# Kernel tuning notes

Hardware: AMD Instinct MI355X
Metric: run time of the kernel (lower is better)

Reference implementation:

```python
import jax, jax.numpy as jnp
import numpy as np

N_NODES = 200000
N_GRAPHS = 512

def gcn_conv(x, src, dst, W, b):
    # PyG GCNConv: add self-loops, symmetric normalization, linear, scatter-add
    n = x.shape[0]
    loop = jnp.arange(n)
    s = jnp.concatenate([src, loop])
    d = jnp.concatenate([dst, loop])
    deg = jax.ops.segment_sum(jnp.ones_like(d, dtype=x.dtype), d, num_segments=n)
    dinv = jnp.where(deg > 0, jax.lax.rsqrt(deg), 0.0)
    norm = dinv[s] * dinv[d]                      # [E+n]
    h = x @ W                                     # [n, out]
    msg = h[s] * norm[:, None]                    # gather on source nodes
    return jax.ops.segment_sum(msg, d, num_segments=n) + b

def setup_inputs() -> dict:
    key = jax.random.key(0)
    ks = jax.random.split(key, 24)
    def g(i, shape, scale=0.05):
        return jax.random.normal(ks[i], shape, dtype=jnp.float32) * scale
    inp = {}
    inp['x'] = jax.random.normal(ks[0], (N_NODES, 78), dtype=jnp.float32)
    inp['edge_index'] = jax.random.randint(ks[1], (2, 800000), 0, N_NODES)
    inp['batch'] = jnp.sort(jax.random.randint(ks[2], (N_NODES,), 0, N_GRAPHS))
    inp['target'] = jax.random.randint(ks[3], (N_GRAPHS, 1000), 0, 26)
    inp['W1'] = g(4, (78, 78)); inp['b1'] = jnp.zeros((78,), jnp.float32)
    inp['W2'] = g(5, (78, 156)); inp['b2'] = jnp.zeros((156,), jnp.float32)
    inp['W3'] = g(6, (156, 312)); inp['b3'] = jnp.zeros((312,), jnp.float32)
    inp['Wg1'] = g(7, (312, 1024)); inp['bg1'] = jnp.zeros((1024,), jnp.float32)
    inp['Wg2'] = g(8, (1024, 128)); inp['bg2'] = jnp.zeros((128,), jnp.float32)
    inp['emb'] = g(9, (26, 128), 1.0)
    inp['convw'] = g(10, (32, 1000, 8))  # OIW
    inp['convb'] = jnp.zeros((32,), jnp.float32)
    inp['Wxt'] = g(11, (32 * 121, 128)); inp['bxt'] = jnp.zeros((128,), jnp.float32)
    inp['Wf1'] = g(12, (256, 1024)); inp['bf1'] = jnp.zeros((1024,), jnp.float32)
    inp['Wf2'] = g(13, (1024, 512)); inp['bf2'] = jnp.zeros((512,), jnp.float32)
    inp['Wo'] = g(14, (512, 1)); inp['bo'] = jnp.zeros((1,), jnp.float32)
    return inp

def reference(x, edge_index, batch, target, W1, b1, W2, b2, W3, b3,
              Wg1, bg1, Wg2, bg2, emb, convw, convb, Wxt, bxt,
              Wf1, bf1, Wf2, bf2, Wo, bo):
    src, dst = edge_index[0], edge_index[1]
    h = jax.nn.relu(gcn_conv(x, src, dst, W1, b1))
    h = jax.nn.relu(gcn_conv(h, src, dst, W2, b2))
    h = jax.nn.relu(gcn_conv(h, src, dst, W3, b3))          # [N, 312]
    g = jax.ops.segment_max(h, batch, num_segments=N_GRAPHS)  # [B, 312]
    g = jnp.where(jnp.isfinite(g), g, 0.0)                   # guard empty segments
    g = jax.nn.relu(g @ Wg1 + bg1)                            # dropout = identity (eval)
    g = g @ Wg2 + bg2                                         # [B, 128]

    e = emb[target]                                           # [B, 1000, 128]
    c = jax.lax.conv_general_dilated(e, convw, (1,), 'VALID',
                                     dimension_numbers=('NCW', 'OIW', 'NCW'))
    c = c + convb[None, :, None]                              # [B, 32, 121]
    xt = c.reshape(-1, 32 * 121) @ Wxt + bxt                  # [B, 128]

    xc = jnp.concatenate([g, xt], axis=1)                     # [B, 256]
    xc = jax.nn.relu(xc @ Wf1 + bf1)
    xc = jax.nn.relu(xc @ Wf2 + bf2)
    return xc @ Wo + bo                                       # [B, 1]
```

## Files before the change

### kernel.cpp

```cpp
#include <hip/hip_runtime.h>
#include <hip/hip_bf16.h>

#define N_NODES 200000
#define N_EDGES 800000
#define N_GRAPHS 512

typedef __attribute__((ext_vector_type(8))) short short8v;
typedef __attribute__((ext_vector_type(4))) float f32x4;
typedef __attribute__((ext_vector_type(2))) float f32x2;
typedef __attribute__((ext_vector_type(2))) unsigned int u32x2;
typedef __attribute__((ext_vector_type(4))) unsigned int u32x4;
typedef __attribute__((ext_vector_type(4))) int i32x4;

__device__ inline float bf2f(unsigned int u) {
    union { unsigned int i; float f; } c;
    c.i = u << 16;
    return c.f;
}
__device__ inline unsigned short f2bf(float f) {
    union { __hip_bfloat16 h; unsigned short u; } c;
    c.h = __float2bfloat16(f);
    return c.u;
}


__global__ __launch_bounds__(256) void count_edges(const int* __restrict__ dst, int E,
                                                   int* __restrict__ cnt) {
    int e = blockIdx.x * 256 + threadIdx.x;
    if (e < E) atomicAdd(&cnt[dst[e]], 1);
}

__global__ __launch_bounds__(512) void block_reduce(const int* __restrict__ in, int n,
                                                    int* __restrict__ bsum) {
    __shared__ int s[512];
    int i = blockIdx.x * 512 + threadIdx.x;
    s[threadIdx.x] = (i < n) ? in[i] : 0;
    __syncthreads();
    for (int off = 256; off; off >>= 1) {
        if (threadIdx.x < off) s[threadIdx.x] += s[threadIdx.x + off];
        __syncthreads();
    }
    if (threadIdx.x == 0) bsum[blockIdx.x] = s[0];
}

__global__ __launch_bounds__(512) void scan_bsums(int* bsum, int nb) {
    __shared__ int buf[2][512];
    int t = threadIdx.x;
    int v = (t < nb) ? bsum[t] : 0;
    buf[0][t] = v;
    __syncthreads();
    int src = 0;
    for (int off = 1; off < 512; off <<= 1) {
        int x = buf[src][t];
        if (t >= off) x += buf[src][t - off];
        buf[src ^ 1][t] = x;
        src ^= 1;
        __syncthreads();
    }
    if (t < nb) bsum[t] = buf[src][t] - v;
}

__global__ __launch_bounds__(512) void block_scan_write(const int* __restrict__ cnt,
                                                        const int* __restrict__ bsum, int n,
                                                        int* __restrict__ rowptr) {
    __shared__ int buf[2][512];
    int t = threadIdx.x;
    int i = blockIdx.x * 512 + t;
    int v = (i < n) ? cnt[i] : 0;
    buf[0][t] = v;
    __syncthreads();
    int src = 0;
    for (int off = 1; off < 512; off <<= 1) {
        int x = buf[src][t];
        if (t >= off) x += buf[src][t - off];
        buf[src ^ 1][t] = x;
        src ^= 1;
        __syncthreads();
    }
    int incl = buf[src][t];
    int base = bsum[blockIdx.x];
    if (i < n) rowptr[i] = base + incl - v;
    if (i == n - 1) rowptr[n] = base + incl;
}

__global__ __launch_bounds__(256) void fill_csr(const int* __restrict__ src,
                                                const int* __restrict__ dst, int E,
                                                const int* __restrict__ rowptr,
                                                int* __restrict__ cur, int* __restrict__ col) {
    int e = blockIdx.x * 256 + threadIdx.x;
    if (e < E) {
        int d = dst[e];
        int p = atomicAdd(&cur[d], 1);
        col[rowptr[d] + p] = src[e];
    }
}

__global__ __launch_bounds__(256) void compute_dinv(const int* __restrict__ rowptr, int n,
                                                    float* __restrict__ dinv) {
    int v = blockIdx.x * 256 + threadIdx.x;
    if (v < n) {
        int deg = rowptr[v + 1] - rowptr[v] + 1;
        dinv[v] = rsqrtf((float)deg);
    }
}

__global__ __launch_bounds__(64) void graph_bounds(const int* __restrict__ batch, int n, int ng,
                                                   int* __restrict__ gstart) {
    int b = blockIdx.x * 64 + threadIdx.x;
    if (b > ng) return;
    if (b == ng) { gstart[ng] = n; return; }
    int lo = 0, hi = n;
    while (lo < hi) {
        int mid = (lo + hi) >> 1;
        if (batch[mid] < b) lo = mid + 1; else hi = mid;
    }
    gstart[b] = lo;
}


__global__ __launch_bounds__(256) void scale_x(const float* __restrict__ x,
                                               const float* __restrict__ dinv,
                                               unsigned short* __restrict__ XS) {
    int idx = blockIdx.x * 256 + threadIdx.x;
    int v = idx / 40, c = idx % 40;
    if (v >= N_NODES) return;
    if (c == 39) {
        *(unsigned int*)(XS + (size_t)v * 80 + 78) = 0u;
        return;
    }
    float dv = dinv[v];
    f32x2 xv = *(const f32x2*)(x + (size_t)v * 78 + c * 2);
    unsigned int pack = ((unsigned int)f2bf(xv.y * dv) << 16) | f2bf(xv.x * dv);
    *(unsigned int*)(XS + (size_t)v * 80 + c * 2) = pack;
}


template <int LD, int NCH, int NPB>
__global__ __launch_bounds__(256) void agg_sum(const unsigned short* __restrict__ X,
                                               const float* __restrict__ dinv,
                                               const int* __restrict__ rowptr,
                                               const int* __restrict__ col,
                                               unsigned short* __restrict__ out) {
    int tid = threadIdx.x;
    if (tid >= NPB * NCH) return;
    int v = blockIdx.x * NPB + tid / NCH;
    int c = tid % NCH;
    if (v >= N_NODES) return;
    u32x4 xv = *(const u32x4*)(X + (size_t)v * LD + c * 8);
    float a0 = bf2f(xv.x & 0xffffu), a1 = bf2f(xv.x >> 16);
    float a2 = bf2f(xv.y & 0xffffu), a3 = bf2f(xv.y >> 16);
    float a4 = bf2f(xv.z & 0xffffu), a5 = bf2f(xv.z >> 16);
    float a6 = bf2f(xv.w & 0xffffu), a7 = bf2f(xv.w >> 16);
    int r0 = rowptr[v], r1 = rowptr[v + 1];
    for (int e = r0; e < r1; ++e) {
        int u = col[e];
        u32x4 xu = *(const u32x4*)(X + (size_t)u * LD + c * 8);
        a0 += bf2f(xu.x & 0xffffu);
        a1 += bf2f(xu.x >> 16);
        a2 += bf2f(xu.y & 0xffffu);
        a3 += bf2f(xu.y >> 16);
        a4 += bf2f(xu.z & 0xffffu);
        a5 += bf2f(xu.z >> 16);
        a6 += bf2f(xu.w & 0xffffu);
        a7 += bf2f(xu.w >> 16);
    }
    float dv = dinv[v];
    u32x4 o;
    o.x = ((unsigned int)f2bf(a1 * dv) << 16) | f2bf(a0 * dv);
    o.y = ((unsigned int)f2bf(a3 * dv) << 16) | f2bf(a2 * dv);
    o.z = ((unsigned int)f2bf(a5 * dv) << 16) | f2bf(a4 * dv);
    o.w = ((unsigned int)f2bf(a7 * dv) << 16) | f2bf(a6 * dv);
    *(u32x4*)(out + (size_t)v * LD + c * 8) = o;
}


template <int KREAL, int NREAL, int KS, int NF>
__global__ __launch_bounds__(256) void prep_wf(const float* __restrict__ W,
                                               unsigned short* __restrict__ Wf) {
    int idx = blockIdx.x * 256 + threadIdx.x;
    if (idx >= NF * KS * 64) return;
    int lane = idx & 63, ks = (idx >> 6) % KS, nf = idx / (64 * KS);
    int k0 = ks * 32 + 8 * (lane >> 4);
    int cc = nf * 16 + (lane & 15);
    short8v t;
#pragma unroll
    for (int j = 0; j < 8; j++) {
        int k = k0 + j;
        float w = (k < KREAL && cc < NREAL) ? W[(size_t)k * NREAL + cc] : 0.f;
        t[j] = (short)f2bf(w);
    }
    *(short8v*)&Wf[(size_t)idx * 8] = t;
}


template <int NREAL, int LDA, int LDC, int NF, int KS>
__global__ __launch_bounds__(256) void gemm_mfma_node(const unsigned short* __restrict__ A,
                                                      const unsigned short* __restrict__ Wf,
                                                      const float* __restrict__ bias,
                                                      const float* __restrict__ dinv,
                                                      unsigned short* __restrict__ Cout, int M) {
    __shared__ unsigned short Bs[NF * KS * 64 * 8];
    int tid = threadIdx.x;
    for (int idx = tid; idx < NF * KS * 64; idx += 256)
        *(short8v*)&Bs[idx * 8] = *(const short8v*)&Wf[(size_t)idx * 8];
    __syncthreads();

    int lane = tid & 63, wid = tid >> 6;
    int m0 = blockIdx.x * 128 + wid * 32;
    float biasr[NF];
#pragma unroll
    for (int nf = 0; nf < NF; nf++) {
        int cc = nf * 16 + (lane & 15);
        biasr[nf] = (cc < NREAL) ? bias[cc] : 0.f;
    }
    f32x4 acc[2][NF];
#pragma unroll
    for (int mf = 0; mf < 2; mf++)
#pragma unroll
        for (int nf = 0; nf < NF; nf++) acc[mf][nf] = (f32x4){0.f, 0.f, 0.f, 0.f};

    int ra = min(m0 + (lane & 15), M - 1);
    int rb = min(m0 + 16 + (lane & 15), M - 1);
#pragma unroll
    for (int ks = 0; ks < KS; ks++) {
        int koff = ks * 32 + 8 * (lane >> 4);
        short8v a0 = *(const short8v*)(A + (size_t)ra * LDA + koff);
        short8v a1 = *(const short8v*)(A + (size_t)rb * LDA + koff);
#pragma unroll
        for (int nf = 0; nf < NF; nf++) {
            short8v b = *(const short8v*)&Bs[((nf * KS + ks) * 64 + lane) * 8];
            acc[0][nf] = __builtin_amdgcn_mfma_f32_16x16x32_bf16(a0, b, acc[0][nf], 0, 0, 0);
            acc[1][nf] = __builtin_amdgcn_mfma_f32_16x16x32_bf16(a1, b, acc[1][nf], 0, 0, 0);
        }
    }
    float dr[2][4];
#pragma unroll
    for (int mf = 0; mf < 2; mf++)
#pragma unroll
        for (int r = 0; r < 4; r++) {
            int row = m0 + mf * 16 + 4 * (lane >> 4) + r;
            dr[mf][r] = dinv[min(row, M - 1)];
        }
#pragma unroll
    for (int mf = 0; mf < 2; mf++) {
#pragma unroll
        for (int nf = 0; nf < NF; nf++) {
            int cc = nf * 16 + (lane & 15);
#pragma unroll
            for (int r = 0; r < 4; r++) {
                int row = m0 + mf * 16 + 4 * (lane >> 4) + r;
                float v = fmaxf(acc[mf][nf][r] + biasr[nf], 0.f) * dr[mf][r];
                unsigned short o = (cc < NREAL) ? f2bf(v) : (unsigned short)0;
                if (row < M) Cout[(size_t)row * LDC + cc] = o;
            }
        }
    }
}


__global__ __launch_bounds__(256) void seg_gemm_max(const unsigned short* __restrict__ A,
                                                    const unsigned short* __restrict__ Wf3,
                                                    const float* __restrict__ b3,
                                                    const int* __restrict__ gstart,
                                                    float* __restrict__ g3) {
    __shared__ unsigned short Bs[4 * 5 * 64 * 8];
    __shared__ float wmax[4][64];
    int g = blockIdx.x & 511;
    int bx = blockIdx.x >> 9;
    int c0 = bx * 64;
    int r0 = gstart[g], r1 = gstart[g + 1];
    int tid = threadIdx.x, lane = tid & 63, wid = tid >> 6;

    const unsigned short* src = Wf3 + (size_t)bx * 4 * 5 * 64 * 8;
    for (int idx = tid; idx < 1280; idx += 256)
        *(short8v*)&Bs[idx * 8] = *(const short8v*)&src[(size_t)idx * 8];
    __syncthreads();

    float biasr[4], cmax[4];
#pragma unroll
    for (int nf = 0; nf < 4; nf++) {
        int cc = c0 + nf * 16 + (lane & 15);
        biasr[nf] = (cc < 312) ? b3[cc] : 0.f;
        cmax[nf] = 0.f;
    }

    for (int mt = r0 + wid * 32; mt < r1; mt += 128) {
        f32x4 acc[2][4];
#pragma unroll
        for (int mf = 0; mf < 2; mf++)
#pragma unroll
            for (int nf = 0; nf < 4; nf++) acc[mf][nf] = (f32x4){0.f, 0.f, 0.f, 0.f};
        int ra = min(mt + (lane & 15), N_NODES - 1);
        int rb = min(mt + 16 + (lane & 15), N_NODES - 1);
#pragma unroll
        for (int ks = 0; ks < 5; ks++) {
            int koff = ks * 32 + 8 * (lane >> 4);
            short8v a0 = *(const short8v*)(A + (size_t)ra * 160 + koff);
            short8v a1 = *(const short8v*)(A + (size_t)rb * 160 + koff);
#pragma unroll
            for (int nf = 0; nf < 4; nf++) {
                short8v b = *(const short8v*)&Bs[((nf * 5 + ks) * 64 + lane) * 8];
                acc[0][nf] = __builtin_amdgcn_mfma_f32_16x16x32_bf16(a0, b, acc[0][nf], 0, 0, 0);
                acc[1][nf] = __builtin_amdgcn_mfma_f32_16x16x32_bf16(a1, b, acc[1][nf], 0, 0, 0);
            }
        }
#pragma unroll
        for (int mf = 0; mf < 2; mf++) {
#pragma unroll
            for (int nf = 0; nf < 4; nf++) {
#pragma unroll
                for (int r = 0; r < 4; r++) {
                    int row = mt + mf * 16 + 4 * (lane >> 4) + r;
                    float v = fmaxf(acc[mf][nf][r] + biasr[nf], 0.f);
                    if (row < r1) cmax[nf] = fmaxf(cmax[nf], v);
                }
            }
        }
    }
#pragma unroll
    for (int nf = 0; nf < 4; nf++) {
        float m = cmax[nf];
        m = fmaxf(m, __shfl_xor(m, 16));
        m = fmaxf(m, __shfl_xor(m, 32));
        if (lane < 16) wmax[wid][nf * 16 + lane] = m;
    }
    __syncthreads();
    if (tid < 64) {
        float m = fmaxf(fmaxf(wmax[0][tid], wmax[1][tid]), fmaxf(wmax[2][tid], wmax[3][tid]));
        int cc = c0 + tid;
        if (cc < 312) g3[(size_t)g * 312 + cc] = m;
    }
}


__global__ __launch_bounds__(256) void init_bias_all(float* __restrict__ gg,
                                                     const float* __restrict__ bg1,
                                                     float* __restrict__ xc,
                                                     const float* __restrict__ bg2,
                                                     const float* __restrict__ bxt,
                                                     float* __restrict__ f1,
                                                     const float* __restrict__ bf1,
                                                     float* __restrict__ f2,
                                                     const float* __restrict__ bf2) {
    int idx = blockIdx.x * 256 + threadIdx.x;
    int row = idx / 2816, c = idx % 2816;
    if (row >= N_GRAPHS) return;
    if (c < 1024) gg[(size_t)row * 1024 + c] = bg1[c];
    else if (c < 1280) {
        int j = c - 1024;
        xc[(size_t)row * 256 + j] = (j < 128) ? bg2[j] : bxt[j - 128];
    } else if (c < 2304)
        f1[(size_t)row * 1024 + (c - 1280)] = bf1[c - 1280];
    else
        f2[(size_t)row * 512 + (c - 2304)] = bf2[c - 2304];
}

template <int RELUA>
__global__ __launch_bounds__(256) void gemm_splitk(const float* __restrict__ A,
                                                   const float* __restrict__ B,
                                                   float* __restrict__ C, int M, int N, int K,
                                                   int ldc, int Kc) {
    __shared__ float As[16][17];
    __shared__ float Bs[16][64];
    int bx = blockIdx.x, by = blockIdx.y, bz = blockIdx.z;
    int tid = threadIdx.x;
    int lane = tid & 63, wy = tid >> 6;
    int n0 = bx * 64, m0 = by * 16;
    int k0 = bz * Kc, k1 = min(K, k0 + Kc);
    float acc[4] = {0.f, 0.f, 0.f, 0.f};
    for (int kt = k0; kt < k1; kt += 16) {
        {
            int r = tid >> 4, kk = tid & 15;
            int gm = m0 + r, gk = kt + kk;
            float v = (gk < k1 && gm < M) ? A[(size_t)gm * K + gk] : 0.f;
            if (RELUA) v = fmaxf(v, 0.f);
            As[kk][r] = v;
        }
#pragma unroll
        for (int l = 0; l < 4; l++) {
            int kk = wy + l * 4;
            int gk = kt + kk, gn = n0 + lane;
            Bs[kk][lane] = (gk < k1 && gn < N) ? B[(size_t)gk * N + gn] : 0.f;
        }
        __syncthreads();
#pragma unroll
        for (int kk = 0; kk < 16; kk++) {
            float b = Bs[kk][lane];
#pragma unroll
            for (int r = 0; r < 4; r++) acc[r] += As[kk][wy * 4 + r] * b;
        }
        __syncthreads();
    }
    int gn = n0 + lane;
    if (gn < N) {
#pragma unroll
        for (int r = 0; r < 4; r++) {
            int gm = m0 + wy * 4 + r;
            if (gm < M) atomicAdd(&C[(size_t)gm * ldc + gn], acc[r]);
        }
    }
}


__global__ __launch_bounds__(256) void prep_cwf(const float* __restrict__ convw,
                                                unsigned short* __restrict__ CWf) {
    int idx = blockIdx.x * 256 + threadIdx.x;
    int ks = idx >> 10, nf = (idx >> 6) & 15, lane = idx & 63;
    int k0 = ks * 32 + 8 * (lane >> 4);
    int c = nf * 16 + (lane & 15);
    int o = c >> 3, kk = c & 7;
    short8v t;
#pragma unroll
    for (int j = 0; j < 8; j++) {
        int k = k0 + j;
        float v = (k < 1000) ? convw[(size_t)o * 8000 + k * 8 + kk] : 0.f;
        t[j] = (short)f2bf(v);
    }
    *(short8v*)&CWf[(size_t)idx * 8] = t;
}

__global__ __launch_bounds__(256) void prep_ef(const float* __restrict__ emb,
                                               unsigned short* __restrict__ Ef) {
    int idx = blockIdx.x * 256 + threadIdx.x;
    if (idx >= 7 * 8 * 64) return;
    int ks = idx >> 9, nf = (idx >> 6) & 7, lane = idx & 63;
    int j0 = ks * 32 + 8 * (lane >> 4);
    int w = nf * 16 + (lane & 15);
    short8v t;
#pragma unroll
    for (int j8 = 0; j8 < 8; j8++) {
        int j = j0 + j8;
        float v = (j < 208 && w < 121) ? emb[(size_t)(j >> 3) * 128 + w + (j & 7)] : 0.f;
        t[j8] = (short)f2bf(v);
    }
    *(short8v*)&Ef[(size_t)idx * 8] = t;
}

__global__ __launch_bounds__(256) void conv_mfma(const int* __restrict__ target,
                                                 const unsigned short* __restrict__ CWf,
                                                 const unsigned short* __restrict__ Ef,
                                                 const float* __restrict__ convb,
                                                 float* __restrict__ c) {
    __shared__ int tg[1024];
    __shared__ unsigned short A_lds[32 * 256];
    int n = blockIdx.x;
    int tid = threadIdx.x, lane = tid & 63, wid = tid >> 6;
    int hi = lane >> 4, l15 = lane & 15;
    for (int i = tid; i < 1024; i += 256) tg[i] = (i < 1000) ? target[n * 1000 + i] : -1;
    __syncthreads();

    f32x4 acc[2][4];
#pragma unroll
    for (int mf = 0; mf < 2; mf++)
#pragma unroll
        for (int nf = 0; nf < 4; nf++) acc[mf][nf] = (f32x4){0.f, 0.f, 0.f, 0.f};
    int r0 = l15, r1 = l15 + 16;
    for (int ks = 0; ks < 32; ks++) {
        int kk = ks * 32 + 8 * hi;
        i32x4 ta = *(const i32x4*)&tg[kk];
        i32x4 tb = *(const i32x4*)&tg[kk + 4];
        short8v a0, a1;
        a0[0] = (ta.x == r0) ? (short)0x3F80 : (short)0;
        a0[1] = (ta.y == r0) ? (short)0x3F80 : (short)0;
        a0[2] = (ta.z == r0) ? (short)0x3F80 : (short)0;
        a0[3] = (ta.w == r0) ? (short)0x3F80 : (short)0;
        a0[4] = (tb.x == r0) ? (short)0x3F80 : (short)0;
        a0[5] = (tb.y == r0) ? (short)0x3F80 : (short)0;
        a0[6] = (tb.z == r0) ? (short)0x3F80 : (short)0;
        a0[7] = (tb.w == r0) ? (short)0x3F80 : (short)0;
        a1[0] = (ta.x == r1) ? (short)0x3F80 : (short)0;
        a1[1] = (ta.y == r1) ? (short)0x3F80 : (short)0;
        a1[2] = (ta.z == r1) ? (short)0x3F80 : (short)0;
        a1[3] = (ta.w == r1) ? (short)0x3F80 : (short)0;
        a1[4] = (tb.x == r1) ? (short)0x3F80 : (short)0;
        a1[5] = (tb.y == r1) ? (short)0x3F80 : (short)0;
        a1[6] = (tb.z == r1) ? (short)0x3F80 : (short)0;
        a1[7] = (tb.w == r1) ? (short)0x3F80 : (short)0;
#pragma unroll
        for (int nf = 0; nf < 4; nf++) {
            short8v b = *(const short8v*)&CWf[((size_t)(ks * 16 + wid * 4 + nf) * 64 + lane) * 8];
            acc[0][nf] = __builtin_amdgcn_mfma_f32_16x16x32_bf16(a0, b, acc[0][nf], 0, 0, 0);
            acc[1][nf] = __builtin_amdgcn_mfma_f32_16x16x32_bf16(a1, b, acc[1][nf], 0, 0, 0);
        }
    }
#pragma unroll
    for (int mf = 0; mf < 2; mf++)
#pragma unroll
        for (int nf = 0; nf < 4; nf++) {
            int col = (wid * 4 + nf) * 16 + l15;
#pragma unroll
            for (int r = 0; r < 4; r++) {
                int row = 16 * mf + 4 * hi + r;
                A_lds[row * 256 + col] = f2bf(acc[mf][nf][r]);
            }
        }
    __syncthreads();

    f32x4 acc2[2][2];
#pragma unroll
    for (int mf = 0; mf < 2; mf++)
#pragma unroll
        for (int nf = 0; nf < 2; nf++) acc2[mf][nf] = (f32x4){0.f, 0.f, 0.f, 0.f};
#pragma unroll
    for (int ks = 0; ks < 7; ks++) {
        int j0 = ks * 32 + 8 * hi;
        int t = j0 >> 3;
        short8v a0 = *(const short8v*)&A_lds[t * 256 + l15 * 8];
        short8v a1 = *(const short8v*)&A_lds[t * 256 + (l15 + 16) * 8];
#pragma unroll
        for (int nf = 0; nf < 2; nf++) {
            short8v b = *(const short8v*)&Ef[((size_t)(ks * 8 + wid * 2 + nf) * 64 + lane) * 8];
            acc2[0][nf] = __builtin_amdgcn_mfma_f32_16x16x32_bf16(a0, b, acc2[0][nf], 0, 0, 0);
            acc2[1][nf] = __builtin_amdgcn_mfma_f32_16x16x32_bf16(a1, b, acc2[1][nf], 0, 0, 0);
        }
    }
#pragma unroll
    for (int mf = 0; mf < 2; mf++)
#pragma unroll
        for (int nf = 0; nf < 2; nf++) {
            int w = (wid * 2 + nf) * 16 + l15;
            if (w < 121) {
#pragma unroll
                for (int r = 0; r < 4; r++) {
                    int o = 16 * mf + 4 * hi + r;
                    c[(size_t)n * 3872 + o * 121 + w] = acc2[mf][nf][r] + convb[o];
                }
            }
        }
}


__global__ __launch_bounds__(256) void rowdot(const float* __restrict__ f2,
                                              const float* __restrict__ Wo,
                                              const float* __restrict__ bo,
                                              float* __restrict__ out, int M, int K) {
    int row = blockIdx.x * 4 + (threadIdx.x >> 6);
    int lane = threadIdx.x & 63;
    if (row >= M) return;
    float acc = 0.f;
    for (int k = lane; k < K; k += 64) acc += fmaxf(f2[(size_t)row * K + k], 0.f) * Wo[k];
    for (int off = 32; off; off >>= 1) acc += __shfl_down(acc, off);
    if (lane == 0) out[row] = acc + bo[0];
}


extern "C" void kernel_launch(void* const* d_in, const int* in_sizes, int n_in, void* d_out,
                              int out_size, void* d_ws, size_t ws_size, hipStream_t stream) {
    const float* x = (const float*)d_in[0];
    const int* ei = (const int*)d_in[1];
    const int* batch = (const int*)d_in[2];
    const int* target = (const int*)d_in[3];
    const float* W1 = (const float*)d_in[4];
    const float* b1 = (const float*)d_in[5];
    const float* W2 = (const float*)d_in[6];
    const float* b2 = (const float*)d_in[7];
    const float* W3 = (const float*)d_in[8];
    const float* b3 = (const float*)d_in[9];
    const float* Wg1 = (const float*)d_in[10];
    const float* bg1 = (const float*)d_in[11];
    const float* Wg2 = (const float*)d_in[12];
    const float* bg2 = (const float*)d_in[13];
    const float* emb = (const float*)d_in[14];
    const float* convw = (const float*)d_in[15];
    const float* convb = (const float*)d_in[16];
    const float* Wxt = (const float*)d_in[17];
    const float* bxt = (const float*)d_in[18];
    const float* Wf1 = (const float*)d_in[19];
    const float* bf1 = (const float*)d_in[20];
    const float* Wf2 = (const float*)d_in[21];
    const float* bf2 = (const float*)d_in[22];
    const float* Wo = (const float*)d_in[23];
    const float* bo = (const float*)d_in[24];
    float* out = (float*)d_out;

    const int N = N_NODES, E = N_EDGES;
    const int NB = (N + 511) / 512;

    char* ws = (char*)d_ws;
    size_t off = 0;
    auto alloc = [&](size_t bytes) -> char* {
        char* p = ws + off;
        off = (off + bytes + 255) & ~(size_t)255;
        return p;
    };
    int* cnt = (int*)alloc((size_t)N * 2 * 4);
    int* cur = cnt + N;
    int* rowptr = (int*)alloc((size_t)(N + 1) * 4);
    int* bsum = (int*)alloc(512 * 4);
    int* col = (int*)alloc((size_t)E * 4);
    float* dinv = (float*)alloc((size_t)N * 4);
    int* gstart = (int*)alloc((N_GRAPHS + 1) * 4);
    float* g3 = (float*)alloc((size_t)N_GRAPHS * 312 * 4);
    float* gg = (float*)alloc((size_t)N_GRAPHS * 1024 * 4);
    float* cbuf = (float*)alloc((size_t)N_GRAPHS * 3872 * 4);
    float* xc = (float*)alloc((size_t)N_GRAPHS * 256 * 4);
    float* f1 = (float*)alloc((size_t)N_GRAPHS * 1024 * 4);
    float* f2 = (float*)alloc((size_t)N_GRAPHS * 512 * 4);
    unsigned short* CWf = (unsigned short*)alloc((size_t)32768 * 8 * 2);
    unsigned short* Ef = (unsigned short*)alloc((size_t)3584 * 8 * 2);
    unsigned short* W1f = (unsigned short*)alloc((size_t)5 * 3 * 64 * 8 * 2);
    unsigned short* W2f = (unsigned short*)alloc((size_t)10 * 3 * 64 * 8 * 2);
    unsigned short* W3f = (unsigned short*)alloc((size_t)20 * 5 * 64 * 8 * 2);
    unsigned short* U = (unsigned short*)alloc((size_t)N * 160 * 2 + 512);
    unsigned short* P160 = (unsigned short*)alloc((size_t)N * 160 * 2 + 512);
    unsigned short* H1 = U + (size_t)N * 80;

    const int* srcp = ei;
    const int* dstp = ei + E;

    hipMemsetAsync(cnt, 0, (size_t)N * 2 * 4, stream);
    count_edges<<<(E + 255) / 256, 256, 0, stream>>>(dstp, E, cnt);
    block_reduce<<<NB, 512, 0, stream>>>(cnt, N, bsum);
    scan_bsums<<<1, 512, 0, stream>>>(bsum, NB);
    block_scan_write<<<NB, 512, 0, stream>>>(cnt, bsum, N, rowptr);
    fill_csr<<<(E + 255) / 256, 256, 0, stream>>>(srcp, dstp, E, rowptr, cur, col);
    compute_dinv<<<(N + 255) / 256, 256, 0, stream>>>(rowptr, N, dinv);
    graph_bounds<<<(N_GRAPHS + 1 + 63) / 64, 64, 0, stream>>>(batch, N, N_GRAPHS, gstart);

    init_bias_all<<<(N_GRAPHS * 2816 + 255) / 256, 256, 0, stream>>>(gg, bg1, xc, bg2, bxt, f1,
                                                                     bf1, f2, bf2);
    prep_cwf<<<128, 256, 0, stream>>>(convw, CWf);
    prep_ef<<<14, 256, 0, stream>>>(emb, Ef);
    prep_wf<78, 78, 3, 5><<<4, 256, 0, stream>>>(W1, W1f);
    prep_wf<78, 156, 3, 10><<<8, 256, 0, stream>>>(W2, W2f);
    prep_wf<156, 312, 5, 20><<<25, 256, 0, stream>>>(W3, W3f);

    const int MB = (N + 127) / 128;

    scale_x<<<(N * 40 + 255) / 256, 256, 0, stream>>>(x, dinv, P160);
    agg_sum<80, 10, 25><<<(N + 24) / 25, 256, 0, stream>>>(P160, dinv, rowptr, col, U);
    gemm_mfma_node<78, 80, 80, 5, 3><<<MB, 256, 0, stream>>>(U, W1f, b1, dinv, H1, N);
    agg_sum<80, 10, 25><<<(N + 24) / 25, 256, 0, stream>>>(H1, dinv, rowptr, col, P160);
    gemm_mfma_node<156, 80, 160, 10, 3><<<MB, 256, 0, stream>>>(P160, W2f, b2, dinv, U, N);
    agg_sum<160, 20, 12><<<(N + 11) / 12, 256, 0, stream>>>(U, dinv, rowptr, col, P160);
    seg_gemm_max<<<5 * N_GRAPHS, 256, 0, stream>>>(P160, W3f, b3, gstart, g3);

    gemm_splitk<0><<<dim3(16, 32, 2), 256, 0, stream>>>(g3, Wg1, gg, 512, 1024, 312, 1024, 160);
    gemm_splitk<1><<<dim3(2, 32, 8), 256, 0, stream>>>(gg, Wg2, xc, 512, 128, 1024, 256, 128);

    conv_mfma<<<N_GRAPHS, 256, 0, stream>>>(target, CWf, Ef, convb, cbuf);
    gemm_splitk<0><<<dim3(2, 32, 16), 256, 0, stream>>>(cbuf, Wxt, xc + 128, 512, 128, 3872, 256, 256);

    gemm_splitk<0><<<dim3(16, 32, 2), 256, 0, stream>>>(xc, Wf1, f1, 512, 1024, 256, 1024, 128);
    gemm_splitk<1><<<dim3(8, 32, 8), 256, 0, stream>>>(f1, Wf2, f2, 512, 512, 1024, 512, 128);
    rowdot<<<(N_GRAPHS + 3) / 4, 256, 0, stream>>>(f2, Wo, bo, out, N_GRAPHS, 512);
}
```

Measured before the change: 690.8 us.

## Merge setup kernels and unroll neighbor aggregation with dual accumulators

```diff
diff --git a/kernel.cpp b/kernel.cpp
--- a/kernel.cpp
+++ b/kernel.cpp
@@ -43,7 +43,22 @@
     if (threadIdx.x == 0) bsum[blockIdx.x] = s[0];
 }
 
-__global__ __launch_bounds__(512) void scan_bsums(int* bsum, int nb) {
+__global__ __launch_bounds__(512) void scan_and_bounds(int* bsum, int nb,
+                                                       const int* __restrict__ batch, int n,
+                                                       int ng, int* __restrict__ gstart) {
+    if (blockIdx.x == 1) {
+        int b = threadIdx.x;
+        if (b == 0) gstart[ng] = n;
+        if (b < ng) {
+            int lo = 0, hi = n;
+            while (lo < hi) {
+                int mid = (lo + hi) >> 1;
+                if (batch[mid] < b) lo = mid + 1; else hi = mid;
+            }
+            gstart[b] = lo;
+        }
+        return;
+    }
     __shared__ int buf[2][512];
     int t = threadIdx.x;
     int v = (t < nb) ? bsum[t] : 0;
@@ -62,7 +77,8 @@
 
 __global__ __launch_bounds__(512) void block_scan_write(const int* __restrict__ cnt,
                                                         const int* __restrict__ bsum, int n,
-                                                        int* __restrict__ rowptr) {
+                                                        int* __restrict__ rowptr,
+                                                        float* __restrict__ dinv) {
     __shared__ int buf[2][512];
     int t = threadIdx.x;
     int i = blockIdx.x * 512 + t;
@@ -79,7 +95,10 @@
     }
     int incl = buf[src][t];
     int base = bsum[blockIdx.x];
-    if (i < n) rowptr[i] = base + incl - v;
+    if (i < n) {
+        rowptr[i] = base + incl - v;
+        dinv[i] = rsqrtf((float)(v + 1));
+    }
     if (i == n - 1) rowptr[n] = base + incl;
 }
 
@@ -93,28 +112,6 @@
         int p = atomicAdd(&cur[d], 1);
         col[rowptr[d] + p] = src[e];
     }
-}
-
-__global__ __launch_bounds__(256) void compute_dinv(const int* __restrict__ rowptr, int n,
-                                                    float* __restrict__ dinv) {
-    int v = blockIdx.x * 256 + threadIdx.x;
-    if (v < n) {
-        int deg = rowptr[v + 1] - rowptr[v] + 1;
-        dinv[v] = rsqrtf((float)deg);
-    }
-}
-
-__global__ __launch_bounds__(64) void graph_bounds(const int* __restrict__ batch, int n, int ng,
-                                                   int* __restrict__ gstart) {
-    int b = blockIdx.x * 64 + threadIdx.x;
-    if (b > ng) return;
-    if (b == ng) { gstart[ng] = n; return; }
-    int lo = 0, hi = n;
-    while (lo < hi) {
-        int mid = (lo + hi) >> 1;
-        if (batch[mid] < b) lo = mid + 1; else hi = mid;
-    }
-    gstart[b] = lo;
 }
 
 
@@ -146,38 +143,60 @@
     int v = blockIdx.x * NPB + tid / NCH;
     int c = tid % NCH;
     if (v >= N_NODES) return;
-    u32x4 xv = *(const u32x4*)(X + (size_t)v * LD + c * 8);
+    const unsigned short* Xc = X + c * 8;
+    u32x4 xv = *(const u32x4*)(Xc + (size_t)v * LD);
     float a0 = bf2f(xv.x & 0xffffu), a1 = bf2f(xv.x >> 16);
     float a2 = bf2f(xv.y & 0xffffu), a3 = bf2f(xv.y >> 16);
     float a4 = bf2f(xv.z & 0xffffu), a5 = bf2f(xv.z >> 16);
     float a6 = bf2f(xv.w & 0xffffu), a7 = bf2f(xv.w >> 16);
+    float b0 = 0.f, b1 = 0.f, b2 = 0.f, b3 = 0.f, b4 = 0.f, b5 = 0.f, b6 = 0.f, b7 = 0.f;
     int r0 = rowptr[v], r1 = rowptr[v + 1];
-    for (int e = r0; e < r1; ++e) {
+    int e = r0;
+    for (; e + 1 < r1; e += 2) {
+        int u0 = col[e], u1 = col[e + 1];
+        u32x4 p = *(const u32x4*)(Xc + (size_t)u0 * LD);
+        u32x4 q = *(const u32x4*)(Xc + (size_t)u1 * LD);
+        a0 += bf2f(p.x & 0xffffu);
+        a1 += bf2f(p.x >> 16);
+        a2 += bf2f(p.y & 0xffffu);
+        a3 += bf2f(p.y >> 16);
+        a4 += bf2f(p.z & 0xffffu);
+        a5 += bf2f(p.z >> 16);
+        a6 += bf2f(p.w & 0xffffu);
+        a7 += bf2f(p.w >> 16);
+        b0 += bf2f(q.x & 0xffffu);
+        b1 += bf2f(q.x >> 16);
+        b2 += bf2f(q.y & 0xffffu);
+        b3 += bf2f(q.y >> 16);
+        b4 += bf2f(q.z & 0xffffu);
+        b5 += bf2f(q.z >> 16);
+        b6 += bf2f(q.w & 0xffffu);
+        b7 += bf2f(q.w >> 16);
+    }
+    if (e < r1) {
         int u = col[e];
-        u32x4 xu = *(const u32x4*)(X + (size_t)u * LD + c * 8);
-        a0 += bf2f(xu.x & 0xffffu);
-        a1 += bf2f(xu.x >> 16);
-        a2 += bf2f(xu.y & 0xffffu);
-        a3 += bf2f(xu.y >> 16);
-        a4 += bf2f(xu.z & 0xffffu);
-        a5 += bf2f(xu.z >> 16);
-        a6 += bf2f(xu.w & 0xffffu);
-        a7 += bf2f(xu.w >> 16);
+        u32x4 p = *(const u32x4*)(Xc + (size_t)u * LD);
+        a0 += bf2f(p.x & 0xffffu);
+        a1 += bf2f(p.x >> 16);
+        a2 += bf2f(p.y & 0xffffu);
+        a3 += bf2f(p.y >> 16);
+        a4 += bf2f(p.z & 0xffffu);
+        a5 += bf2f(p.z >> 16);
+        a6 += bf2f(p.w & 0xffffu);
+        a7 += bf2f(p.w >> 16);
     }
     float dv = dinv[v];
     u32x4 o;
-    o.x = ((unsigned int)f2bf(a1 * dv) << 16) | f2bf(a0 * dv);
-    o.y = ((unsigned int)f2bf(a3 * dv) << 16) | f2bf(a2 * dv);
-    o.z = ((unsigned int)f2bf(a5 * dv) << 16) | f2bf(a4 * dv);
-    o.w = ((unsigned int)f2bf(a7 * dv) << 16) | f2bf(a6 * dv);
+    o.x = ((unsigned int)f2bf((a1 + b1) * dv) << 16) | f2bf((a0 + b0) * dv);
+    o.y = ((unsigned int)f2bf((a3 + b3) * dv) << 16) | f2bf((a2 + b2) * dv);
+    o.z = ((unsigned int)f2bf((a5 + b5) * dv) << 16) | f2bf((a4 + b4) * dv);
+    o.w = ((unsigned int)f2bf((a7 + b7) * dv) << 16) | f2bf((a6 + b6) * dv);
     *(u32x4*)(out + (size_t)v * LD + c * 8) = o;
 }
 
 
-template <int KREAL, int NREAL, int KS, int NF>
-__global__ __launch_bounds__(256) void prep_wf(const float* __restrict__ W,
-                                               unsigned short* __restrict__ Wf) {
-    int idx = blockIdx.x * 256 + threadIdx.x;
+__device__ inline void prep_wf_body(const float* __restrict__ W, unsigned short* __restrict__ Wf,
+                                    int idx, int KREAL, int NREAL, int KS, int NF) {
     if (idx >= NF * KS * 64) return;
     int lane = idx & 63, ks = (idx >> 6) % KS, nf = idx / (64 * KS);
     int k0 = ks * 32 + 8 * (lane >> 4);
@@ -190,6 +209,73 @@
         t[j] = (short)f2bf(w);
     }
     *(short8v*)&Wf[(size_t)idx * 8] = t;
+}
+
+__global__ __launch_bounds__(256) void setup_misc(
+    float* __restrict__ gg, const float* __restrict__ bg1, float* __restrict__ xc,
+    const float* __restrict__ bg2, const float* __restrict__ bxt, float* __restrict__ f1,
+    const float* __restrict__ bf1, float* __restrict__ f2, const float* __restrict__ bf2,
+    const float* __restrict__ convw, unsigned short* __restrict__ CWf,
+    const float* __restrict__ emb, unsigned short* __restrict__ Ef,
+    const float* __restrict__ W1, unsigned short* __restrict__ W1f,
+    const float* __restrict__ W2, unsigned short* __restrict__ W2f,
+    const float* __restrict__ W3, unsigned short* __restrict__ W3f) {
+    int b = blockIdx.x;
+    int tid = threadIdx.x;
+    if (b < 5632) {
+        int idx = b * 256 + tid;
+        int row = idx / 2816, c = idx % 2816;
+        if (row >= N_GRAPHS) return;
+        if (c < 1024) gg[(size_t)row * 1024 + c] = bg1[c];
+        else if (c < 1280) {
+            int j = c - 1024;
+            xc[(size_t)row * 256 + j] = (j < 128) ? bg2[j] : bxt[j - 128];
+        } else if (c < 2304)
+            f1[(size_t)row * 1024 + (c - 1280)] = bf1[c - 1280];
+        else
+            f2[(size_t)row * 512 + (c - 2304)] = bf2[c - 2304];
+        return;
+    }
+    b -= 5632;
+    if (b < 128) {
+        int idx = b * 256 + tid;
+        int ks = idx >> 10, nf = (idx >> 6) & 15, lane = idx & 63;
+        int k0 = ks * 32 + 8 * (lane >> 4);
+        int c = nf * 16 + (lane & 15);
+        int o = c >> 3, kk = c & 7;
+        short8v t;
+#pragma unroll
+        for (int j = 0; j < 8; j++) {
+            int k = k0 + j;
+            float v = (k < 1000) ? convw[(size_t)o * 8000 + k * 8 + kk] : 0.f;
+            t[j] = (short)f2bf(v);
+        }
+        *(short8v*)&CWf[(size_t)idx * 8] = t;
+        return;
+    }
+    b -= 128;
+    if (b < 14) {
+        int idx = b * 256 + tid;
+        if (idx >= 7 * 8 * 64) return;
+        int ks = idx >> 9, nf = (idx >> 6) & 7, lane = idx & 63;
+        int j0 = ks * 32 + 8 * (lane >> 4);
+        int w = nf * 16 + (lane & 15);
+        short8v t;
+#pragma unroll
+        for (int j8 = 0; j8 < 8; j8++) {
+            int j = j0 + j8;
+            float v = (j < 208 && w < 121) ? emb[(size_t)(j >> 3) * 128 + w + (j & 7)] : 0.f;
+            t[j8] = (short)f2bf(v);
+        }
+        *(short8v*)&Ef[(size_t)idx * 8] = t;
+        return;
+    }
+    b -= 14;
+    if (b < 4) { prep_wf_body(W1, W1f, b * 256 + tid, 78, 78, 3, 5); return; }
+    b -= 4;
+    if (b < 8) { prep_wf_body(W2, W2f, b * 256 + tid, 78, 156, 3, 10); return; }
+    b -= 8;
+    prep_wf_body(W3, W3f, b * 256 + tid, 156, 312, 5, 20);
 }
 
 
@@ -332,28 +418,6 @@
     }
 }
 
-
-__global__ __launch_bounds__(256) void init_bias_all(float* __restrict__ gg,
-                                                     const float* __restrict__ bg1,
-                                                     float* __restrict__ xc,
-                                                     const float* __restrict__ bg2,
-                                                     const float* __restrict__ bxt,
-                                                     float* __restrict__ f1,
-                                                     const float* __restrict__ bf1,
-                                                     float* __restrict__ f2,
-                                                     const float* __restrict__ bf2) {
-    int idx = blockIdx.x * 256 + threadIdx.x;
-    int row = idx / 2816, c = idx % 2816;
-    if (row >= N_GRAPHS) return;
-    if (c < 1024) gg[(size_t)row * 1024 + c] = bg1[c];
-    else if (c < 1280) {
-        int j = c - 1024;
-        xc[(size_t)row * 256 + j] = (j < 128) ? bg2[j] : bxt[j - 128];
-    } else if (c < 2304)
-        f1[(size_t)row * 1024 + (c - 1280)] = bf1[c - 1280];
-    else
-        f2[(size_t)row * 512 + (c - 2304)] = bf2[c - 2304];
-}
 
 template <int RELUA>
 __global__ __launch_bounds__(256) void gemm_splitk(const float* __restrict__ A,
@@ -401,40 +465,6 @@
     }
 }
 
-
-__global__ __launch_bounds__(256) void prep_cwf(const float* __restrict__ convw,
-                                                unsigned short* __restrict__ CWf) {
-    int idx = blockIdx.x * 256 + threadIdx.x;
-    int ks = idx >> 10, nf = (idx >> 6) & 15, lane = idx & 63;
-    int k0 = ks * 32 + 8 * (lane >> 4);
-    int c = nf * 16 + (lane & 15);
-    int o = c >> 3, kk = c & 7;
-    short8v t;
-#pragma unroll
-    for (int j = 0; j < 8; j++) {
-        int k = k0 + j;
-        float v = (k < 1000) ? convw[(size_t)o * 8000 + k * 8 + kk] : 0.f;
-        t[j] = (short)f2bf(v);
-    }
-    *(short8v*)&CWf[(size_t)idx * 8] = t;
-}
-
-__global__ __launch_bounds__(256) void prep_ef(const float* __restrict__ emb,
-                                               unsigned short* __restrict__ Ef) {
-    int idx = blockIdx.x * 256 + threadIdx.x;
-    if (idx >= 7 * 8 * 64) return;
-    int ks = idx >> 9, nf = (idx >> 6) & 7, lane = idx & 63;
-    int j0 = ks * 32 + 8 * (lane >> 4);
-    int w = nf * 16 + (lane & 15);
-    short8v t;
-#pragma unroll
-    for (int j8 = 0; j8 < 8; j8++) {
-        int j = j0 + j8;
-        float v = (j < 208 && w < 121) ? emb[(size_t)(j >> 3) * 128 + w + (j & 7)] : 0.f;
-        t[j8] = (short)f2bf(v);
-    }
-    *(short8v*)&Ef[(size_t)idx * 8] = t;
-}
 
 __global__ __launch_bounds__(256) void conv_mfma(const int* __restrict__ target,
                                                  const unsigned short* __restrict__ CWf,
@@ -611,19 +641,12 @@
     hipMemsetAsync(cnt, 0, (size_t)N * 2 * 4, stream);
     count_edges<<<(E + 255) / 256, 256, 0, stream>>>(dstp, E, cnt);
     block_reduce<<<NB, 512, 0, stream>>>(cnt, N, bsum);
-    scan_bsums<<<1, 512, 0, stream>>>(bsum, NB);
-    block_scan_write<<<NB, 512, 0, stream>>>(cnt, bsum, N, rowptr);
+    scan_and_bounds<<<2, 512, 0, stream>>>(bsum, NB, batch, N, N_GRAPHS, gstart);
+    block_scan_write<<<NB, 512, 0, stream>>>(cnt, bsum, N, rowptr, dinv);
     fill_csr<<<(E + 255) / 256, 256, 0, stream>>>(srcp, dstp, E, rowptr, cur, col);
-    compute_dinv<<<(N + 255) / 256, 256, 0, stream>>>(rowptr, N, dinv);
-    graph_bounds<<<(N_GRAPHS + 1 + 63) / 64, 64, 0, stream>>>(batch, N, N_GRAPHS, gstart);
-
-    init_bias_all<<<(N_GRAPHS * 2816 + 255) / 256, 256, 0, stream>>>(gg, bg1, xc, bg2, bxt, f1,
-                                                                     bf1, f2, bf2);
-    prep_cwf<<<128, 256, 0, stream>>>(convw, CWf);
-    prep_ef<<<14, 256, 0, stream>>>(emb, Ef);
-    prep_wf<78, 78, 3, 5><<<4, 256, 0, stream>>>(W1, W1f);
-    prep_wf<78, 156, 3, 10><<<8, 256, 0, stream>>>(W2, W2f);
-    prep_wf<156, 312, 5, 20><<<25, 256, 0, stream>>>(W3, W3f);
+
+    setup_misc<<<5632 + 128 + 14 + 4 + 8 + 25, 256, 0, stream>>>(
+        gg, bg1, xc, bg2, bxt, f1, bf1, f2, bf2, convw, CWf, emb, Ef, W1, W1f, W2, W2f, W3, W3f);
 
     const int MB = (N + 127) / 128;
 
```

Result: faster. 664.1 us (-3.9%).
